# Performance work log

Measured on AMD Instinct MI355X. Metric: run time of the kernel, lower is better.

The kernel has to match this reference:

```python
import jax, jax.numpy as jnp
import numpy as np

N, E = 50000, 600000
DIN, DMID, DATTR, DOUT, DEMB, DH, K = 128, 128, 32, 128, 256, 768, 16


def setup_inputs() -> dict:
    key = jax.random.key(0)
    ks = jax.random.split(key, 12)
    s = lambda d: 1.0 / np.sqrt(d)
    return {
        "x": jax.random.normal(ks[0], (N, DIN), jnp.float32),
        "attributes": jax.random.normal(ks[1], (N, DATTR), jnp.float32),
        "edge_weight": jax.random.uniform(ks[2], (E,), jnp.float32),
        "hidden_state": jax.random.normal(ks[3], (1, DH), jnp.float32),
        "edge_index": jax.random.randint(ks[4], (2, E), 0, N, jnp.int64),
        "W1": jax.random.normal(ks[5], (DIN, DMID), jnp.float32) * s(DIN),
        "b1": jnp.zeros((DMID,), jnp.float32),
        "W2": jax.random.normal(ks[6], (DMID + DATTR, DOUT), jnp.float32) * s(DMID + DATTR),
        "b2": jnp.zeros((DOUT,), jnp.float32),
        "Wmap": jax.random.normal(ks[7], (DOUT + DATTR, DEMB), jnp.float32) * s(DOUT + DATTR),
        "bmap": jnp.zeros((DEMB,), jnp.float32),
        "Wattn": jax.random.normal(ks[8], (DH, DOUT + DATTR), jnp.float32) * s(DH),
    }


def gcn_conv(x, W, b, src, dst, w, n):
    """PyG GCNConv with normalize=True: A_hat = D^-1/2 (A+I) D^-1/2, out = A_hat X W + b."""
    loop = jnp.arange(n, dtype=src.dtype)
    src2 = jnp.concatenate([src, loop])
    dst2 = jnp.concatenate([dst, loop])
    w2 = jnp.concatenate([w, jnp.ones((n,), x.dtype)])
    deg = jax.ops.segment_sum(w2, dst2, num_segments=n)
    dinv = jnp.where(deg > 0, jax.lax.rsqrt(jnp.maximum(deg, 1e-12)), 0.0)
    norm = dinv[src2] * w2 * dinv[dst2]        # [E+N]
    h = x @ W                                   # [n, out] transform first (small dim)
    msg = h[src2] * norm[:, None]               # gather + scale, [E+N, out]
    return jax.ops.segment_sum(msg, dst2, num_segments=n) + b


def reference(x, attributes, edge_weight, hidden_state, edge_index,
              W1, b1, W2, b2, Wmap, bmap, Wattn):
    n = x.shape[0]
    src, dst = edge_index[0], edge_index[1]
    h = jax.nn.relu(gcn_conv(x, W1, b1, src, dst, edge_weight, n))
    # F.dropout with training=False is identity (module run in eval mode)
    h = jnp.concatenate([h, attributes], axis=1)           # [N, DMID+DATTR]
    h = gcn_conv(h, W2, b2, src, dst, edge_weight, n)      # [N, DOUT]
    h = jnp.concatenate([h, attributes], axis=1)           # [N, DOUT+DATTR]
    # DotAttnChoseImportentNode: project hidden state, dot with node feats, take top-K nodes
    q = hidden_state @ Wattn                                # [1, DOUT+DATTR]
    scores = h @ q[0]                                       # [N]
    _, idx = jax.lax.top_k(scores, K)
    chose_nodes = h[idx].reshape(1, -1)                     # [1, K*(DOUT+DATTR)]
    # final_mapping: mean-pool graph embed + linear
    emb = jnp.mean(h, axis=0, keepdims=True) @ Wmap + bmap  # [1, DEMB]
    return jnp.concatenate([emb, chose_nodes], axis=1)      # [1, DEMB + K*(DOUT+DATTR)]
```

## Files before the change

### kernel.cpp

```cpp
#include <hip/hip_runtime.h>

#define N_NODES 50000
#define N_EDGES 600000
#define D_IN 128
#define D_MID 128
#define D_ATTR 32
#define D_OUT 128
#define D_EMB 256
#define D_H 768
#define K_TOP 16
#define D_CAT (D_OUT + D_ATTR)
#define N_CHUNKBLKS 196
#define N_CAND (N_CHUNKBLKS * K_TOP)
#define CSLOTS 13
#define WSCALE 262144.0f
#define CS_BLOCKS 768

__global__ void k_init(unsigned long long* packed, float* q) {
    int i = blockIdx.x * blockDim.x + threadIdx.x;
    if (i < N_NODES) packed[i] = 0ULL;
    if (i < D_CAT)   q[i] = 0.0f;
}

__global__ void k_deg(const int* __restrict__ dst, const float* __restrict__ w,
                      unsigned long long* __restrict__ packed) {
    int e = blockIdx.x * blockDim.x + threadIdx.x;
    if (e < N_EDGES) {
        int d = dst[e];
        unsigned long long q = (1ULL << 40)
                             + (unsigned long long)__float2uint_rn(w[e] * WSCALE);
        atomicAdd(&packed[d], q);
    }
}

__global__ void k_dinv(const unsigned long long* __restrict__ packed,
                       float* __restrict__ dinv, int* __restrict__ counts) {
    int i = blockIdx.x * blockDim.x + threadIdx.x;
    if (i < N_NODES) {
        unsigned long long p = packed[i];
        counts[i] = (int)(p >> 40);
        float wsum = (float)(p & 0xFFFFFFFFFFULL) * (1.0f / WSCALE);
        dinv[i] = rsqrtf(1.0f + wsum);
    }
}

__global__ __launch_bounds__(256) void k_scan_blk(const int* __restrict__ counts,
                                                  int* __restrict__ incl,
                                                  int* __restrict__ bsum) {
    __shared__ int sm[256];
    int tid = threadIdx.x;
    int i = blockIdx.x * 256 + tid;
    int v = (i < N_NODES) ? counts[i] : 0;
    sm[tid] = v;
    __syncthreads();
    for (int off = 1; off < 256; off <<= 1) {
        int t = (tid >= off) ? sm[tid - off] : 0;
        __syncthreads();
        sm[tid] += t;
        __syncthreads();
    }
    if (i < N_NODES) incl[i] = sm[tid];
    if (tid == 255) bsum[blockIdx.x] = sm[255];
}

__global__ __launch_bounds__(256) void k_scan_top(const int* __restrict__ bsum,
                                                  int* __restrict__ boff) {
    __shared__ int sm[256];
    int tid = threadIdx.x;
    int v = (tid < N_CHUNKBLKS) ? bsum[tid] : 0;
    sm[tid] = v;
    __syncthreads();
    for (int off = 1; off < 256; off <<= 1) {
        int t = (tid >= off) ? sm[tid - off] : 0;
        __syncthreads();
        sm[tid] += t;
        __syncthreads();
    }
    if (tid < N_CHUNKBLKS) boff[tid] = sm[tid] - v;
}

__global__ __launch_bounds__(256) void k_scan_add(const int* __restrict__ incl,
                                                  const int* __restrict__ boff,
                                                  const int* __restrict__ counts,
                                                  int* __restrict__ row_ptr,
                                                  int* __restrict__ cursor) {
    int i = blockIdx.x * 256 + threadIdx.x;
    if (i < N_NODES) {
        int ip = incl[i] + boff[blockIdx.x];
        row_ptr[i + 1] = ip;
        cursor[i] = ip - counts[i];
        if (i == 0) row_ptr[0] = 0;
    }
}

__global__ void k_fill(const int* __restrict__ src, const int* __restrict__ dst,
                       const float* __restrict__ w, const float* __restrict__ dinv,
                       int* __restrict__ cursor, int2* __restrict__ recs) {
    int e = blockIdx.x * blockDim.x + threadIdx.x;
    if (e < N_EDGES) {
        int s = src[e], d = dst[e];
        int pos = atomicAdd(&cursor[d], 1);
        float nr = dinv[s] * w[e] * dinv[d];
        recs[pos] = make_int2(s, __float_as_int(nr));
    }
}

#define GBM 128
#define GBK 32
__global__ __launch_bounds__(256) void k_gemm(
    const float* __restrict__ in1, int d1,
    const float* __restrict__ in2, int d2,
    const float* __restrict__ W,
    float* __restrict__ out)
{
    __shared__ float xs[GBM][GBK + 1];
    __shared__ float ws[GBK][128];
    int tid = threadIdx.x;
    int cx = tid & 7;
    int ry = tid >> 3;
    int row0 = blockIdx.x * GBM;
    float acc[4][16];
#pragma unroll
    for (int i = 0; i < 4; ++i)
#pragma unroll
        for (int j = 0; j < 16; ++j) acc[i][j] = 0.0f;
    int KD = d1 + d2;
    for (int kt = 0; kt < KD; kt += GBK) {
        const float* srcp; int sd, scol;
        if (kt < d1) { srcp = in1; sd = d1; scol = kt; }
        else         { srcp = in2; sd = d2; scol = kt - d1; }
#pragma unroll
        for (int i = 0; i < 4; ++i) {
            int vid = tid + i * 256;
            int rr = vid >> 3;
            int kc = (vid & 7) * 4;
            int r = row0 + rr;
            float4 val = make_float4(0.f, 0.f, 0.f, 0.f);
            if (r < N_NODES)
                val = *(const float4*)(srcp + (size_t)r * sd + scol + kc);
            xs[rr][kc + 0] = val.x;
            xs[rr][kc + 1] = val.y;
            xs[rr][kc + 2] = val.z;
            xs[rr][kc + 3] = val.w;
        }
#pragma unroll
        for (int i = 0; i < 4; ++i) {
            int vid = tid + i * 256;
            int kk = vid >> 5;
            int c = (vid & 31) * 4;
            *(float4*)&ws[kk][c] = *(const float4*)(W + (size_t)(kt + kk) * 128 + c);
        }
        __syncthreads();
#pragma unroll
        for (int kk = 0; kk < GBK; ++kk) {
            float xv[4];
#pragma unroll
            for (int i = 0; i < 4; ++i) xv[i] = xs[ry * 4 + i][kk];
            float wv[16];
            *(float4*)&wv[0]  = *(float4*)&ws[kk][cx * 16 + 0];
            *(float4*)&wv[4]  = *(float4*)&ws[kk][cx * 16 + 4];
            *(float4*)&wv[8]  = *(float4*)&ws[kk][cx * 16 + 8];
            *(float4*)&wv[12] = *(float4*)&ws[kk][cx * 16 + 12];
#pragma unroll
            for (int i = 0; i < 4; ++i)
#pragma unroll
                for (int j = 0; j < 16; ++j)
                    acc[i][j] += xv[i] * wv[j];
        }
        __syncthreads();
    }
#pragma unroll
    for (int i = 0; i < 4; ++i) {
        int r = row0 + ry * 4 + i;
        if (r < N_NODES) {
            float4* o = (float4*)(out + (size_t)r * 128 + cx * 16);
            o[0] = *(float4*)&acc[i][0];
            o[1] = *(float4*)&acc[i][4];
            o[2] = *(float4*)&acc[i][8];
            o[3] = *(float4*)&acc[i][12];
        }
    }
}

__global__ __launch_bounds__(256) void k_agg(
    const float* __restrict__ t, const float* __restrict__ dinv,
    const int* __restrict__ row_ptr, const int2* __restrict__ recs,
    const float* __restrict__ bias,
    float* __restrict__ out, int relu_flag,
    const float* __restrict__ attr, const float* __restrict__ q,
    float* __restrict__ scores, int score_flag)
{
    int lane = threadIdx.x & 31;
    int node = blockIdx.x * 8 + (threadIdx.x >> 5);
    if (node >= N_NODES) return;
    const float4* t4 = (const float4*)t;
    float di = dinv[node];
    float sw = di * di;
    float4 v = t4[node * 32 + lane];
    float4 acc;
    acc.x = v.x * sw; acc.y = v.y * sw; acc.z = v.z * sw; acc.w = v.w * sw;
    int e0 = row_ptr[node], e1 = row_ptr[node + 1];
    for (int e = e0; e < e1; ++e) {
        int2 rec = recs[e];
        int s = rec.x;
        float wn = __int_as_float(rec.y);
        float4 u = t4[s * 32 + lane];
        acc.x += wn * u.x; acc.y += wn * u.y; acc.z += wn * u.z; acc.w += wn * u.w;
    }
    const float4* b4 = (const float4*)bias;
    float4 bb = b4[lane];
    acc.x += bb.x; acc.y += bb.y; acc.z += bb.z; acc.w += bb.w;
    if (relu_flag) {
        acc.x = fmaxf(acc.x, 0.0f); acc.y = fmaxf(acc.y, 0.0f);
        acc.z = fmaxf(acc.z, 0.0f); acc.w = fmaxf(acc.w, 0.0f);
    }
    ((float4*)out)[node * 32 + lane] = acc;
    if (score_flag) {
        const float4* q4 = (const float4*)q;
        float4 qq = q4[lane];
        float s = acc.x * qq.x + acc.y * qq.y + acc.z * qq.z + acc.w * qq.w;
        if (lane < 8) {
            const float4* at4 = (const float4*)attr;
            float4 b = at4[node * 8 + lane];
            float4 q2 = q4[32 + lane];
            s += b.x * q2.x + b.y * q2.y + b.z * q2.z + b.w * q2.w;
        }
        for (int off = 16; off; off >>= 1) s += __shfl_xor(s, off, 32);
        if (lane == 0) scores[node] = s;
    }
}

__global__ void k_q(const float* __restrict__ hs, const float* __restrict__ Wattn,
                    float* __restrict__ q) {
    int j = threadIdx.x;
    if (j >= D_CAT) return;
    int k0 = blockIdx.x * (D_H / 8);
    float acc = 0.0f;
    for (int k = k0; k < k0 + D_H / 8; k++) acc += hs[k] * Wattn[k * D_CAT + j];
    atomicAdd(&q[j], acc);
}

__global__ __launch_bounds__(256) void k_colsum_partial(const float* __restrict__ h2,
                                                        const float* __restrict__ attr,
                                                        float* __restrict__ partial) {
    __shared__ float4 sm[256];
    int tid = threadIdx.x;
    int per = (N_NODES + CS_BLOCKS - 1) / CS_BLOCKS;
    int r0 = blockIdx.x * per;
    int r1 = min(N_NODES, r0 + per);
    float* myrow = partial + (size_t)blockIdx.x * D_CAT;
    {
        const float4* h4 = (const float4*)h2;
        int c = tid & 31;
        float4 acc = make_float4(0.f, 0.f, 0.f, 0.f);
        for (int r = r0 + (tid >> 5); r < r1; r += 8) {
            float4 v = h4[(size_t)r * 32 + c];
            acc.x += v.x; acc.y += v.y; acc.z += v.z; acc.w += v.w;
        }
        sm[tid] = acc;
        __syncthreads();
        if (tid < 32) {
            float4 s = sm[tid];
#pragma unroll
            for (int g = 1; g < 8; ++g) {
                float4 v = sm[g * 32 + tid];
                s.x += v.x; s.y += v.y; s.z += v.z; s.w += v.w;
            }
            ((float4*)myrow)[tid] = s;
        }
        __syncthreads();
    }
    {
        const float4* a4 = (const float4*)attr;
        int c = tid & 7;
        float4 acc = make_float4(0.f, 0.f, 0.f, 0.f);
        for (int r = r0 + (tid >> 3); r < r1; r += 32) {
            float4 v = a4[(size_t)r * 8 + c];
            acc.x += v.x; acc.y += v.y; acc.z += v.z; acc.w += v.w;
        }
        sm[tid] = acc;
        __syncthreads();
        if (tid < 8) {
            float4 s = sm[tid];
#pragma unroll
            for (int g = 1; g < 32; ++g) {
                float4 v = sm[g * 8 + tid];
                s.x += v.x; s.y += v.y; s.z += v.z; s.w += v.w;
            }
            ((float4*)(myrow + D_OUT))[tid] = s;
        }
    }
}

__global__ __launch_bounds__(256) void k_colsum_reduce(const float* __restrict__ partial,
                                                       float* __restrict__ colsum) {
    __shared__ float4 sm[256];
    int tid = threadIdx.x;
    int cg = blockIdx.x;
    float4 acc = make_float4(0.f, 0.f, 0.f, 0.f);
#pragma unroll
    for (int k = 0; k < 3; ++k) {
        int b = tid + k * 256;
        float4 v = *(const float4*)(partial + (size_t)b * D_CAT + cg * 4);
        acc.x += v.x; acc.y += v.y; acc.z += v.z; acc.w += v.w;
    }
    sm[tid] = acc;
    __syncthreads();
    for (int off = 128; off; off >>= 1) {
        if (tid < off) {
            float4 v = sm[tid + off];
            sm[tid].x += v.x; sm[tid].y += v.y; sm[tid].z += v.z; sm[tid].w += v.w;
        }
        __syncthreads();
    }
    if (tid == 0) *(float4*)(colsum + cg * 4) = sm[0];
}

__global__ __launch_bounds__(256) void k_top1(const float* __restrict__ scores,
                                              float* __restrict__ cand_s,
                                              int* __restrict__ cand_i) {
    __shared__ float ss[256];
    __shared__ int si[256];
    __shared__ float rs[256];
    __shared__ int ri[256];
    int tid = threadIdx.x;
    int i = blockIdx.x * 256 + tid;
    ss[tid] = (i < N_NODES) ? scores[i] : -INFINITY;
    si[tid] = i;
    __syncthreads();
    for (int it = 0; it < K_TOP; ++it) {
        rs[tid] = ss[tid]; ri[tid] = si[tid];
        __syncthreads();
        for (int off = 128; off; off >>= 1) {
            if (tid < off) {
                float s2 = rs[tid + off]; int i2 = ri[tid + off];
                if (s2 > rs[tid] || (s2 == rs[tid] && i2 < ri[tid])) { rs[tid] = s2; ri[tid] = i2; }
            }
            __syncthreads();
        }
        if (tid == 0) {
            cand_s[blockIdx.x * K_TOP + it] = rs[0];
            cand_i[blockIdx.x * K_TOP + it] = ri[0];
        }
        __syncthreads();
        if (si[tid] == ri[0]) ss[tid] = -INFINITY;
        __syncthreads();
    }
}

__global__ __launch_bounds__(256) void k_top2(const float* __restrict__ cand_s,
                                              const int* __restrict__ cand_i,
                                              int* __restrict__ topidx) {
    float s[CSLOTS]; int ix[CSLOTS];
    int tid = threadIdx.x;
    int lane = tid & 63;
    int wave = tid >> 6;
#pragma unroll
    for (int j = 0; j < CSLOTS; ++j) {
        int c = tid + j * 256;
        s[j]  = (c < N_CAND) ? cand_s[c] : -INFINITY;
        ix[j] = (c < N_CAND) ? cand_i[c] : 0x7fffffff;
    }
    __shared__ float wsum_s[4];
    __shared__ int   wsum_i[4];
    __shared__ int   win_i;
    for (int it = 0; it < K_TOP; ++it) {
        float bs = -INFINITY; int bi = 0x7fffffff;
#pragma unroll
        for (int j = 0; j < CSLOTS; ++j) {
            if (s[j] > bs || (s[j] == bs && ix[j] < bi)) { bs = s[j]; bi = ix[j]; }
        }
#pragma unroll
        for (int off = 32; off; off >>= 1) {
            float s2 = __shfl_xor(bs, off, 64);
            int   i2 = __shfl_xor(bi, off, 64);
            if (s2 > bs || (s2 == bs && i2 < bi)) { bs = s2; bi = i2; }
        }
        if (lane == 0) { wsum_s[wave] = bs; wsum_i[wave] = bi; }
        __syncthreads();
        if (tid == 0) {
            float ws0 = wsum_s[0]; int wi0 = wsum_i[0];
#pragma unroll
            for (int w = 1; w < 4; ++w) {
                float s2 = wsum_s[w]; int i2 = wsum_i[w];
                if (s2 > ws0 || (s2 == ws0 && i2 < wi0)) { ws0 = s2; wi0 = i2; }
            }
            win_i = wi0;
            topidx[it] = wi0;
        }
        __syncthreads();
        int w = win_i;
#pragma unroll
        for (int j = 0; j < CSLOTS; ++j)
            if (ix[j] == w) s[j] = -INFINITY;
        __syncthreads();
    }
}

__global__ __launch_bounds__(256) void k_emb_gather(
    const float* __restrict__ colsum, const float* __restrict__ Wmap,
    const float* __restrict__ bmap, const int* __restrict__ topidx,
    const float* __restrict__ h2, const float* __restrict__ attr,
    float* __restrict__ out)
{
    int tid = threadIdx.x;
    __shared__ float cs[D_CAT];
    if (tid < D_CAT) cs[tid] = colsum[tid];
    __syncthreads();
    float acc = 0.0f;
#pragma unroll 8
    for (int k = 0; k < D_CAT; ++k) acc += cs[k] * Wmap[k * D_EMB + tid];
    out[tid] = acc * (1.0f / N_NODES) + bmap[tid];
    __shared__ int ti[K_TOP];
    if (tid < K_TOP) ti[tid] = topidx[tid];
    __syncthreads();
    for (int idx = tid; idx < K_TOP * D_CAT; idx += 256) {
        int kk = idx / D_CAT;
        int d = idx % D_CAT;
        int node = ti[kk];
        out[D_EMB + idx] = (d < D_OUT) ? h2[node * D_OUT + d]
                                       : attr[node * D_ATTR + (d - D_OUT)];
    }
}

extern "C" void kernel_launch(void* const* d_in, const int* in_sizes, int n_in,
                              void* d_out, int out_size, void* d_ws, size_t ws_size,
                              hipStream_t stream) {
    const float* x      = (const float*)d_in[0];
    const float* attr   = (const float*)d_in[1];
    const float* ew     = (const float*)d_in[2];
    const float* hs     = (const float*)d_in[3];
    const int*   ei     = (const int*)d_in[4];
    const float* W1     = (const float*)d_in[5];
    const float* b1     = (const float*)d_in[6];
    const float* W2     = (const float*)d_in[7];
    const float* b2     = (const float*)d_in[8];
    const float* Wmap   = (const float*)d_in[9];
    const float* bmap   = (const float*)d_in[10];
    const float* Wattn  = (const float*)d_in[11];
    float* out = (float*)d_out;
    const int* e_src = ei;
    const int* e_dst = ei + N_EDGES;

    size_t off = 0;
    auto alloc = [&](size_t bytes) {
        void* p = (char*)d_ws + off;
        off += (bytes + 255) / 256 * 256;
        return p;
    };
    unsigned long long* packed = (unsigned long long*)alloc((size_t)N_NODES * 8);
    float* dinv   = (float*)alloc((size_t)N_NODES * 4);
    int*   counts = (int*)  alloc((size_t)N_NODES * 4);
    int*   rowp   = (int*)  alloc((size_t)(N_NODES + 1) * 4);
    int*   cursor = (int*)  alloc((size_t)N_NODES * 4);
    int2*  recs   = (int2*) alloc((size_t)N_EDGES * 8);
    float* bufA   = (float*)alloc((size_t)N_NODES * 128 * 4);
    float* bufB   = (float*)alloc((size_t)N_NODES * 128 * 4);
    float* scores = (float*)alloc((size_t)N_NODES * 4);
    float* q      = (float*)alloc(D_CAT * 4);
    float* colsum = (float*)alloc(D_CAT * 4);
    float* partial= (float*)alloc((size_t)CS_BLOCKS * D_CAT * 4);
    float* cand_s = (float*)alloc((size_t)N_CAND * 4);
    int*   cand_i = (int*)  alloc((size_t)N_CAND * 4);
    int*   incl   = (int*)  alloc((size_t)N_NODES * 4);
    int*   bsum   = (int*)  alloc((size_t)N_CHUNKBLKS * 4);
    int*   boff   = (int*)  alloc((size_t)N_CHUNKBLKS * 4);
    int*   topidx = (int*)  alloc((size_t)K_TOP * 4);

    int nblk = (N_NODES + 255) / 256;
    int eblk = (N_EDGES + 255) / 256;

    hipLaunchKernelGGL(k_init, dim3(nblk), dim3(256), 0, stream, packed, q);
    hipLaunchKernelGGL(k_deg, dim3(eblk), dim3(256), 0, stream, e_dst, ew, packed);
    hipLaunchKernelGGL(k_dinv, dim3(nblk), dim3(256), 0, stream, packed, dinv, counts);
    hipLaunchKernelGGL(k_scan_blk, dim3(nblk), dim3(256), 0, stream, counts, incl, bsum);
    hipLaunchKernelGGL(k_scan_top, dim3(1), dim3(256), 0, stream, bsum, boff);
    hipLaunchKernelGGL(k_scan_add, dim3(nblk), dim3(256), 0, stream, incl, boff, counts,
                       rowp, cursor);
    hipLaunchKernelGGL(k_fill, dim3(eblk), dim3(256), 0, stream, e_src, e_dst, ew, dinv,
                       cursor, recs);
    hipLaunchKernelGGL(k_q, dim3(8), dim3(192), 0, stream, hs, Wattn, q);
    hipLaunchKernelGGL(k_gemm, dim3((N_NODES + GBM - 1) / GBM), dim3(256), 0, stream,
                       x, D_IN, x, 0, W1, bufA);
    hipLaunchKernelGGL(k_agg, dim3(N_NODES / 8), dim3(256), 0, stream,
                       bufA, dinv, rowp, recs, b1, bufB, 1,
                       (const float*)nullptr, (const float*)nullptr, (float*)nullptr, 0);
    hipLaunchKernelGGL(k_gemm, dim3((N_NODES + GBM - 1) / GBM), dim3(256), 0, stream,
                       bufB, D_MID, attr, D_ATTR, W2, bufA);
    hipLaunchKernelGGL(k_agg, dim3(N_NODES / 8), dim3(256), 0, stream,
                       bufA, dinv, rowp, recs, b2, bufB, 0,
                       attr, q, scores, 1);
    hipLaunchKernelGGL(k_colsum_partial, dim3(CS_BLOCKS), dim3(256), 0, stream,
                       bufB, attr, partial);
    hipLaunchKernelGGL(k_colsum_reduce, dim3(D_CAT / 4), dim3(256), 0, stream,
                       partial, colsum);
    hipLaunchKernelGGL(k_top1, dim3(N_CHUNKBLKS), dim3(256), 0, stream,
                       scores, cand_s, cand_i);
    hipLaunchKernelGGL(k_top2, dim3(1), dim3(256), 0, stream, cand_s, cand_i, topidx);
    hipLaunchKernelGGL(k_emb_gather, dim3(1), dim3(256), 0, stream,
                       colsum, Wmap, bmap, topidx, bufB, attr, out);
}
```

Before: 335.9 us.

## Use one full 64-lane wavefront per node in GCN aggregation with shuffled edge records

The aggregation kernel now maps one 64-wide wavefront to each node instead of a 32-lane half-wave. Each lane handles a float2 of the 128 features. Edge records are loaded cooperatively, one per lane, then broadcast with shuffles. The inner loop is unrolled by four so several neighbor-row gathers are in flight at once. This is meant to cut redundant per-lane record loads and raise memory-level parallelism on the irregular gathers. In exchange it uses narrower per-lane loads and extra shuffle instructions.

```diff
diff --git a/kernel.cpp b/kernel.cpp
--- a/kernel.cpp
+++ b/kernel.cpp
@@ -190,42 +190,65 @@
     const float* __restrict__ attr, const float* __restrict__ q,
     float* __restrict__ scores, int score_flag)
 {
-    int lane = threadIdx.x & 31;
-    int node = blockIdx.x * 8 + (threadIdx.x >> 5);
+    int lane = threadIdx.x & 63;
+    int node = blockIdx.x * 4 + (threadIdx.x >> 6);
     if (node >= N_NODES) return;
-    const float4* t4 = (const float4*)t;
+    const float2* t2 = (const float2*)t;
     float di = dinv[node];
     float sw = di * di;
-    float4 v = t4[node * 32 + lane];
-    float4 acc;
-    acc.x = v.x * sw; acc.y = v.y * sw; acc.z = v.z * sw; acc.w = v.w * sw;
+    float2 v = t2[(size_t)node * 64 + lane];
+    float accx = v.x * sw, accy = v.y * sw;
     int e0 = row_ptr[node], e1 = row_ptr[node + 1];
-    for (int e = e0; e < e1; ++e) {
-        int2 rec = recs[e];
-        int s = rec.x;
-        float wn = __int_as_float(rec.y);
-        float4 u = t4[s * 32 + lane];
-        acc.x += wn * u.x; acc.y += wn * u.y; acc.z += wn * u.z; acc.w += wn * u.w;
-    }
-    const float4* b4 = (const float4*)bias;
-    float4 bb = b4[lane];
-    acc.x += bb.x; acc.y += bb.y; acc.z += bb.z; acc.w += bb.w;
+    int len = e1 - e0;
+    for (int base = 0; base < len; base += 64) {
+        int m = len - base; if (m > 64) m = 64;
+        int2 myrec = make_int2(0, 0);
+        if (lane < m) myrec = recs[e0 + base + lane];
+        int j = 0;
+        for (; j + 4 <= m; j += 4) {
+            int s0 = __shfl(myrec.x, j + 0, 64);
+            int s1 = __shfl(myrec.x, j + 1, 64);
+            int s2 = __shfl(myrec.x, j + 2, 64);
+            int s3 = __shfl(myrec.x, j + 3, 64);
+            float w0 = __int_as_float(__shfl(myrec.y, j + 0, 64));
+            float w1 = __int_as_float(__shfl(myrec.y, j + 1, 64));
+            float w2 = __int_as_float(__shfl(myrec.y, j + 2, 64));
+            float w3 = __int_as_float(__shfl(myrec.y, j + 3, 64));
+            float2 u0 = t2[(size_t)s0 * 64 + lane];
+            float2 u1 = t2[(size_t)s1 * 64 + lane];
+            float2 u2 = t2[(size_t)s2 * 64 + lane];
+            float2 u3 = t2[(size_t)s3 * 64 + lane];
+            accx += w0 * u0.x + w1 * u1.x + w2 * u2.x + w3 * u3.x;
+            accy += w0 * u0.y + w1 * u1.y + w2 * u2.y + w3 * u3.y;
+        }
+        for (; j < m; ++j) {
+            int s = __shfl(myrec.x, j, 64);
+            float wn = __int_as_float(__shfl(myrec.y, j, 64));
+            float2 u = t2[(size_t)s * 64 + lane];
+            accx += wn * u.x;
+            accy += wn * u.y;
+        }
+    }
+    const float2* b2 = (const float2*)bias;
+    float2 bb = b2[lane];
+    accx += bb.x; accy += bb.y;
     if (relu_flag) {
-        acc.x = fmaxf(acc.x, 0.0f); acc.y = fmaxf(acc.y, 0.0f);
-        acc.z = fmaxf(acc.z, 0.0f); acc.w = fmaxf(acc.w, 0.0f);
-    }
-    ((float4*)out)[node * 32 + lane] = acc;
+        accx = fmaxf(accx, 0.0f);
+        accy = fmaxf(accy, 0.0f);
+    }
+    float2 res; res.x = accx; res.y = accy;
+    ((float2*)out)[(size_t)node * 64 + lane] = res;
     if (score_flag) {
-        const float4* q4 = (const float4*)q;
-        float4 qq = q4[lane];
-        float s = acc.x * qq.x + acc.y * qq.y + acc.z * qq.z + acc.w * qq.w;
-        if (lane < 8) {
-            const float4* at4 = (const float4*)attr;
-            float4 b = at4[node * 8 + lane];
-            float4 q2 = q4[32 + lane];
-            s += b.x * q2.x + b.y * q2.y + b.z * q2.z + b.w * q2.w;
-        }
-        for (int off = 16; off; off >>= 1) s += __shfl_xor(s, off, 32);
+        const float2* q2 = (const float2*)q;
+        float2 qq = q2[lane];
+        float s = accx * qq.x + accy * qq.y;
+        if (lane < 16) {
+            const float2* at2 = (const float2*)attr;
+            float2 a = at2[(size_t)node * 16 + lane];
+            float2 qa = q2[64 + lane];
+            s += a.x * qa.x + a.y * qa.y;
+        }
+        for (int off = 32; off; off >>= 1) s += __shfl_xor(s, off, 64);
         if (lane == 0) scores[node] = s;
     }
 }
@@ -482,12 +505,12 @@
     hipLaunchKernelGGL(k_q, dim3(8), dim3(192), 0, stream, hs, Wattn, q);
     hipLaunchKernelGGL(k_gemm, dim3((N_NODES + GBM - 1) / GBM), dim3(256), 0, stream,
                        x, D_IN, x, 0, W1, bufA);
-    hipLaunchKernelGGL(k_agg, dim3(N_NODES / 8), dim3(256), 0, stream,
+    hipLaunchKernelGGL(k_agg, dim3((N_NODES + 3) / 4), dim3(256), 0, stream,
                        bufA, dinv, rowp, recs, b1, bufB, 1,
                        (const float*)nullptr, (const float*)nullptr, (float*)nullptr, 0);
     hipLaunchKernelGGL(k_gemm, dim3((N_NODES + GBM - 1) / GBM), dim3(256), 0, stream,
                        bufB, D_MID, attr, D_ATTR, W2, bufA);
-    hipLaunchKernelGGL(k_agg, dim3(N_NODES / 8), dim3(256), 0, stream,
+    hipLaunchKernelGGL(k_agg, dim3((N_NODES + 3) / 4), dim3(256), 0, stream,
                        bufA, dinv, rowp, recs, b2, bufB, 0,
                        attr, q, scores, 1);
     hipLaunchKernelGGL(k_colsum_partial, dim3(CS_BLOCKS), dim3(256), 0, stream,
```

Measured after the change: 324.6 us. -3.4%, faster.
